# Kernel tuning notes

Hardware: AMD Instinct MI355X
Metric: run time of the kernel (lower is better)

## Reference

```python
import jax, jax.numpy as jnp
import numpy as np

B, L, V = 128, 48, 32000
NUM_BRANCHES, BRANCH_SIZE = 16, 8  # branch_nums = [8]*16, sum == B


def setup_inputs() -> dict:
    key = jax.random.key(0)
    k1, k2 = jax.random.split(key)
    tgt_tokens = jax.random.randint(k1, (B, L), 0, V, dtype=jnp.int32)
    pred = jax.random.normal(k2, (B, L, V), dtype=jnp.float32)
    # segment id per sample, encoding branch_nums = [BRANCH_SIZE]*NUM_BRANCHES
    seg_ids = jnp.repeat(jnp.arange(NUM_BRANCHES, dtype=jnp.int32), BRANCH_SIZE)
    return {"tgt_tokens": tgt_tokens, "pred": pred, "seg_ids": seg_ids}


def reference(tgt_tokens, pred, seg_ids):
    # batched cross-entropy with ignore_index=-100 (mean over valid tokens per sample)
    logp = jax.nn.log_softmax(pred, axis=-1)                      # [B, L, V]
    valid = tgt_tokens != -100                                    # [B, L]
    tok = jnp.where(valid, tgt_tokens, 0)
    nll = -jnp.take_along_axis(logp, tok[..., None], axis=-1)[..., 0]
    nll = jnp.where(valid, nll, 0.0)
    count = valid.sum(axis=-1).astype(pred.dtype)                 # valid tokens per sample
    ce_losses = nll.sum(axis=-1) / count                          # [B]
    # seq_probs[i] = exp(-count_i * ce_i) == exp(sum of token log-probs)
    seq_probs = jnp.exp(-count * ce_losses)                       # [B] (detached in original)
    # per-branch: -log(mean(exp(-ce)))  == -(logsumexp(-ce) - log(branch_num))
    neg = -ce_losses
    m = jax.ops.segment_max(neg, seg_ids, num_segments=NUM_BRANCHES)
    s = jax.ops.segment_sum(jnp.exp(neg - m[seg_ids]), seg_ids, num_segments=NUM_BRANCHES)
    cnt = jax.ops.segment_sum(jnp.ones_like(neg), seg_ids, num_segments=NUM_BRANCHES)
    branch_loss = -(jnp.log(s) + m - jnp.log(cnt))                # [NUM_BRANCHES]
    loss = jnp.mean(branch_loss)
    return loss, jax.lax.stop_gradient(seq_probs)
```

## Files before the change

### kernel.cpp

```cpp
#include <hip/hip_runtime.h>
#include <math.h>

#define BB 128
#define LL 48
#define VV 32000
#define NSEG 16

typedef float v4f __attribute__((ext_vector_type(4)));

__global__ __launch_bounds__(256, 8) void row_nll_kernel(
    const int* __restrict__ tgt, const float* __restrict__ pred,
    float* __restrict__ nll_ws)
{
    const int wave = threadIdx.x >> 6;
    const int lane = threadIdx.x & 63;
    const int row  = blockIdx.x * 2 + (wave >> 1);
    const int half = wave & 1;
    const float* __restrict__ p = pred + (size_t)row * VV;

    const int t = tgt[row];
    const float tlogit = (t != -100) ? p[t] : 0.0f;

    const v4f* __restrict__ p4 = (const v4f*)p;
    float s0 = 0.0f, s1 = 0.0f, s2 = 0.0f, s3 = 0.0f;
    #pragma unroll 4
    for (int i = lane + 64 * half; i < VV / 4; i += 128) {
        v4f v = __builtin_nontemporal_load(&p4[i]);
        s0 += __expf(v.x);
        s1 += __expf(v.y);
        s2 += __expf(v.z);
        s3 += __expf(v.w);
    }
    float s = (s0 + s1) + (s2 + s3);

    #pragma unroll
    for (int off = 1; off < 64; off <<= 1)
        s += __shfl_xor(s, off);

    __shared__ float sw[4];
    if (lane == 0) sw[wave] = s;
    __syncthreads();

    if (lane == 0 && half == 0) {
        float tot = sw[wave] + sw[wave + 1];
        nll_ws[row] = (t != -100) ? (logf(tot) - tlogit) : 0.0f;
    }
}

__global__ __launch_bounds__(128) void finalize_kernel(
    const int* __restrict__ tgt, const int* __restrict__ seg_ids,
    const float* __restrict__ nll_ws, float* __restrict__ out)
{
    const int b = threadIdx.x;

    __shared__ float nl[BB * LL];
    __shared__ int   tg[BB * LL];
    for (int idx = b; idx < BB * LL; idx += 128) {
        nl[idx] = nll_ws[idx];
        tg[idx] = tgt[idx];
    }
    __syncthreads();

    float sum = 0.0f; int count = 0;
    for (int l = 0; l < LL; l++) {
        sum += nl[b * LL + l];
        if (tg[b * LL + l] != -100) count++;
    }
    float ce = sum / (float)count;
    out[1 + b] = expf(-sum);

    __shared__ float neg[BB];
    __shared__ int   seg[BB];
    __shared__ float bl[NSEG];
    neg[b] = -ce;
    seg[b] = seg_ids[b];
    __syncthreads();

    if (b < NSEG) {
        float m = -INFINITY;
        for (int i = 0; i < BB; i++)
            if (seg[i] == b) m = fmaxf(m, neg[i]);
        float ssum = 0.0f; int cnt = 0;
        for (int i = 0; i < BB; i++)
            if (seg[i] == b) { ssum += expf(neg[i] - m); cnt++; }
        bl[b] = -(logf(ssum) + m - logf((float)cnt));
    }
    __syncthreads();

    if (b == 0) {
        float loss = 0.0f;
        for (int i = 0; i < NSEG; i++) loss += bl[i];
        out[0] = loss / (float)NSEG;
    }
}

extern "C" void kernel_launch(void* const* d_in, const int* in_sizes, int n_in,
                              void* d_out, int out_size, void* d_ws, size_t ws_size,
                              hipStream_t stream) {
    const int*   tgt  = (const int*)d_in[0];
    const float* pred = (const float*)d_in[1];
    const int*   seg  = (const int*)d_in[2];
    float* out    = (float*)d_out;
    float* nll_ws = (float*)d_ws;

    row_nll_kernel<<<(BB * LL) / 2, 256, 0, stream>>>(tgt, pred, nll_ws);
    finalize_kernel<<<1, BB, 0, stream>>>(tgt, seg, nll_ws, out);
}
```

Measured before the change: 147.2 us.

## Assign one wave per row and batch ten vector loads before exp

Each wave now handles a full vocabulary row instead of two waves splitting one, which removes the shared-memory exchange and block barrier. The inner loop is rewritten to issue ten nontemporal vec4 loads into registers before doing the exps, giving more memory-level parallelism per wave. The loop is fully specialized to the fixed vocabulary size. In exchange it raises register use, drops the occupancy hint, and halves the number of blocks in flight.

```diff
diff --git a/kernel.cpp b/kernel.cpp
--- a/kernel.cpp
+++ b/kernel.cpp
@@ -8,14 +8,13 @@
 
 typedef float v4f __attribute__((ext_vector_type(4)));
 
-__global__ __launch_bounds__(256, 8) void row_nll_kernel(
+__global__ __launch_bounds__(256) void row_nll_kernel(
     const int* __restrict__ tgt, const float* __restrict__ pred,
     float* __restrict__ nll_ws)
 {
     const int wave = threadIdx.x >> 6;
     const int lane = threadIdx.x & 63;
-    const int row  = blockIdx.x * 2 + (wave >> 1);
-    const int half = wave & 1;
+    const int row  = blockIdx.x * 4 + wave;
     const float* __restrict__ p = pred + (size_t)row * VV;
 
     const int t = tgt[row];
@@ -23,13 +22,31 @@
 
     const v4f* __restrict__ p4 = (const v4f*)p;
     float s0 = 0.0f, s1 = 0.0f, s2 = 0.0f, s3 = 0.0f;
-    #pragma unroll 4
-    for (int i = lane + 64 * half; i < VV / 4; i += 128) {
-        v4f v = __builtin_nontemporal_load(&p4[i]);
-        s0 += __expf(v.x);
-        s1 += __expf(v.y);
-        s2 += __expf(v.z);
-        s3 += __expf(v.w);
+
+    int i = lane;
+    v4f buf[10];
+    for (int c = 0; c < 12; ++c) {
+        #pragma unroll
+        for (int u = 0; u < 10; ++u)
+            buf[u] = __builtin_nontemporal_load(&p4[i + u * 64]);
+        #pragma unroll
+        for (int u = 0; u < 10; ++u) {
+            s0 += __expf(buf[u].x);
+            s1 += __expf(buf[u].y);
+            s2 += __expf(buf[u].z);
+            s3 += __expf(buf[u].w);
+        }
+        i += 640;
+    }
+    #pragma unroll
+    for (int u = 0; u < 5; ++u)
+        buf[u] = __builtin_nontemporal_load(&p4[i + u * 64]);
+    #pragma unroll
+    for (int u = 0; u < 5; ++u) {
+        s0 += __expf(buf[u].x);
+        s1 += __expf(buf[u].y);
+        s2 += __expf(buf[u].z);
+        s3 += __expf(buf[u].w);
     }
     float s = (s0 + s1) + (s2 + s3);
 
@@ -37,13 +54,9 @@
     for (int off = 1; off < 64; off <<= 1)
         s += __shfl_xor(s, off);
 
-    __shared__ float sw[4];
-    if (lane == 0) sw[wave] = s;
-    __syncthreads();
-
-    if (lane == 0 && half == 0) {
-        float tot = sw[wave] + sw[wave + 1];
-        nll_ws[row] = (t != -100) ? (logf(tot) - tlogit) : 0.0f;
+    if (lane == 0) {
+        float nll = (t != -100) ? (logf(s) - tlogit) : 0.0f;
+        nll_ws[row] = nll;
     }
 }
 
@@ -103,6 +116,6 @@
     float* out    = (float*)d_out;
     float* nll_ws = (float*)d_ws;
 
-    row_nll_kernel<<<(BB * LL) / 2, 256, 0, stream>>>(tgt, pred, nll_ws);
+    row_nll_kernel<<<(BB * LL) / 4, 256, 0, stream>>>(tgt, pred, nll_ws);
     finalize_kernel<<<1, BB, 0, stream>>>(tgt, seg, nll_ws, out);
 }
```

Measured after the change: 146.5 us. Within noise of the previous version (-0.5%).
